# Optimization experiments

Measured on AMD Instinct MI355X. Metric: run time of the kernel, lower is better.

## Reference

```python
import jax, jax.numpy as jnp
import numpy as np

B, J, O = 32, 20, 20
D, H, F, L = 256, 8, 1024, 6
S = J * O
DH = D // H
NL = L + 1  # 6 encoder blocks + final block stacked together


def setup_inputs() -> dict:
    ks = jax.random.split(jax.random.key(0), 16)
    s = 0.02
    am = jax.random.randint(ks[4], (B, J), 0, 2) == 1
    am = am.at[:, 0].set(False)  # at least one unmasked job per row (avoid all -inf softmax)
    return {
        "operations": jax.random.normal(ks[0], (B, J, O, 2), jnp.float32),
        "job_ops_mask": jax.random.normal(ks[1], (B, J, O, O), jnp.float32),
        "ops_machines_mask": jax.random.normal(ks[2], (B, S, S), jnp.float32),
        "jobs_next_op_idx": jax.random.randint(ks[3], (B, J, 1), 0, O),
        "action_mask": am,
        "qkv_w": jax.random.normal(ks[5], (NL, 3 * D, D), jnp.float32) * s,
        "qkv_b": jnp.zeros((NL, 3 * D), jnp.float32),
        "out_w": jax.random.normal(ks[6], (NL, D, D), jnp.float32) * s,
        "out_b": jnp.zeros((NL, D), jnp.float32),
        "ln1_g": jnp.ones((NL, D), jnp.float32),
        "ln1_b": jnp.zeros((NL, D), jnp.float32),
        "ln2_g": jnp.ones((NL, D), jnp.float32),
        "ln2_b": jnp.zeros((NL, D), jnp.float32),
        "ff1_w": jax.random.normal(ks[7], (NL, F, D), jnp.float32) * s,
        "ff1_b": jnp.zeros((NL, F), jnp.float32),
        "ff2_w": jax.random.normal(ks[8], (NL, D, F), jnp.float32) * s,
        "ff2_b": jnp.zeros((NL, D), jnp.float32),
        "op_emb_w": jax.random.normal(ks[9], (D, 2), jnp.float32) * s,
        "op_emb_b": jnp.zeros((D,), jnp.float32),
        "pol_w": jax.random.normal(ks[10], (1, D), jnp.float32) * s,
        "pol_b": jnp.zeros((1,), jnp.float32),
    }


def _ln(x, g, b):
    m = x.mean(-1, keepdims=True)
    v = ((x - m) ** 2).mean(-1, keepdims=True)
    return (x - m) * jax.lax.rsqrt(v + 1e-5) * g + b


def _mha(x, mask, qw, qb, ow, ob):
    N, Sq, _ = x.shape
    qkv = x @ qw.T + qb
    q, k, v = jnp.split(qkv, 3, axis=-1)
    q = q.reshape(N, Sq, H, DH).transpose(0, 2, 1, 3)
    k = k.reshape(N, Sq, H, DH).transpose(0, 2, 1, 3)
    v = v.reshape(N, Sq, H, DH).transpose(0, 2, 1, 3)
    sc = jnp.einsum("nhqd,nhkd->nhqk", q, k) / jnp.sqrt(jnp.float32(DH))
    sc = sc + mask  # additive float attn mask, broadcast over heads where needed
    a = jax.nn.softmax(sc, axis=-1)
    o = jnp.einsum("nhqk,nhkd->nhqd", a, v).transpose(0, 2, 1, 3).reshape(N, Sq, D)
    return o @ ow.T + ob


def _forward(operations, job_ops_mask, ops_machines_mask, jobs_next_op_idx, action_mask,
             qkv_w, qkv_b, out_w, out_b, ln1_g, ln1_b, ln2_g, ln2_b,
             ff1_w, ff1_b, ff2_w, ff2_b, op_emb_w, op_emb_b, pol_w, pol_b):
    def block(x, mask, i):  # pre-norm TransformerEncoderLayer, gelu, dropout=0
        h = _ln(x, ln1_g[i], ln1_b[i])
        x = x + _mha(h, mask, qkv_w[i], qkv_b[i], out_w[i], out_b[i])
        h = _ln(x, ln2_g[i], ln2_b[i])
        ff = jax.nn.gelu(h @ ff1_w[i].T + ff1_b[i], approximate=False) @ ff2_w[i].T + ff2_b[i]
        return x + ff

    # sinusoidal positional encoding over the operation index
    pos = jnp.arange(O, dtype=jnp.float32)[:, None]
    div = jnp.exp(jnp.arange(0, D, 2, dtype=jnp.float32) * (-np.log(10000.0) / D))
    pe = jnp.stack([jnp.sin(pos * div), jnp.cos(pos * div)], axis=-1).reshape(O, D)
    x = operations @ op_emb_w.T + op_emb_b + pe[None, None]  # (B,J,O,D)

    # ALiBi slopes: 1/x^(i+1), x = 256^(1/H)
    base = (2.0 ** 8) ** (1.0 / H)
    slope = (1.0 / base ** jnp.arange(1, H + 1, dtype=jnp.float32))[None, :, None, None]
    job_mask = job_ops_mask.reshape(B * J, 1, O, O) * slope  # (B*J, H, O, O)
    mach_mask = ops_machines_mask[:, None, :, :]  # (B, 1, S, S), identical across heads

    for i in range(L):
        if i % 2 == 0:  # per-job attention over operations
            x = block(x.reshape(B * J, O, D), job_mask, i).reshape(B, J, O, D)
        else:  # per-machine attention over all operations
            x = block(x.reshape(B, S, D), mach_mask, i).reshape(B, J, O, D)

    idx = jnp.broadcast_to(jobs_next_op_idx[:, :, :, None], (B, J, 1, D))
    nxt = jnp.take_along_axis(x, idx, axis=2)[:, :, 0, :]  # (B, J, D)
    kp = jnp.where(action_mask, -jnp.inf, 0.0)[:, None, None, :]  # key padding mask
    nxt = block(nxt, kp, L)
    logits = (nxt @ pol_w.T + pol_b)[:, :, 0]
    return jnp.where(action_mask, -jnp.inf, logits)


def reference(operations, job_ops_mask, ops_machines_mask, jobs_next_op_idx, action_mask,
              qkv_w, qkv_b, out_w, out_b, ln1_g, ln1_b, ln2_g, ln2_b,
              ff1_w, ff1_b, ff2_w, ff2_b, op_emb_w, op_emb_b, pol_w, pol_b):
    return _forward(operations, job_ops_mask, ops_machines_mask, jobs_next_op_idx, action_mask,
                    qkv_w, qkv_b, out_w, out_b, ln1_g, ln1_b, ln2_g, ln2_b,
                    ff1_w, ff1_b, ff2_w, ff2_b, op_emb_w, op_emb_b, pol_w, pol_b)
```

## Files before the change

### kernel.cpp

```cpp
#include <hip/hip_runtime.h>
#include <math.h>

#define B_  32
#define J_  20
#define O_  20
#define S_  400
#define D_  256
#define H_  8
#define F_  1024
#define L_  6
#define T_  12800
#define T2_ 640

#define NEG_BIG (-1e30f)

typedef __attribute__((ext_vector_type(8))) short short8;
typedef __attribute__((ext_vector_type(4))) float f32x4;

__device__ __forceinline__ short f2b(float f) {
  union { float f; unsigned u; } c; c.f = f;
  unsigned r = (c.u + 0x7FFFu + ((c.u >> 16) & 1u)) >> 16;
  return (short)r;
}
__device__ __forceinline__ float b2f(short s) {
  union { unsigned u; float f; } c;
  c.u = ((unsigned)(unsigned short)s) << 16;
  return c.f;
}
__device__ __forceinline__ unsigned addpk(unsigned a, unsigned b) {
  union { unsigned u; float f; } x, y;
  x.u = a << 16;        y.u = b << 16;        float lo = x.f + y.f;
  x.u = a & 0xffff0000u; y.u = b & 0xffff0000u; float hi = x.f + y.f;
  return (unsigned)(unsigned short)f2b(lo) | ((unsigned)(unsigned short)f2b(hi) << 16);
}
__device__ __forceinline__ void async_copy16(const short* g, short* l) {
  __builtin_amdgcn_global_load_lds(
      (const __attribute__((address_space(1))) void*)g,
      (__attribute__((address_space(3))) void*)l, 16, 0, 0);
}

__global__ __launch_bounds__(256) void k_f2b4(
    const float* __restrict__ s0, short* __restrict__ d0,
    const float* __restrict__ s1, short* __restrict__ d1,
    const float* __restrict__ s2, short* __restrict__ d2,
    const float* __restrict__ s3, short* __restrict__ d3,
    const float* __restrict__ s4, short* __restrict__ d4)
{
  int bid = blockIdx.x;
  const float* src; short* dst; int base;
  if (bid < 672)        { src = s0; dst = d0; base = bid; }
  else if (bid < 896)   { src = s1; dst = d1; base = bid - 672; }
  else if (bid < 1792)  { src = s2; dst = d2; base = bid - 896; }
  else if (bid < 2688)  { src = s3; dst = d3; base = bid - 1792; }
  else                  { src = s4; dst = d4; base = bid - 2688; }
  int i = (base * 256 + threadIdx.x) * 8;
  float4 a = *(const float4*)(src + i);
  float4 b = *(const float4*)(src + i + 4);
  short8 o;
  o[0] = f2b(a.x); o[1] = f2b(a.y); o[2] = f2b(a.z); o[3] = f2b(a.w);
  o[4] = f2b(b.x); o[5] = f2b(b.y); o[6] = f2b(b.z); o[7] = f2b(b.w);
  *(short8*)(dst + i) = o;
}

__global__ __launch_bounds__(640) void k_maskconv(
    const void* __restrict__ am_raw, int* __restrict__ am_out)
{
  __shared__ int isInt32;
  const int tid = threadIdx.x;
  if (tid == 0) isInt32 = 1;
  __syncthreads();
  if (tid < 160) {
    int v = ((const int*)am_raw)[tid];
    if (v != 0 && v != 1) atomicAnd(&isInt32, 0);
  }
  __syncthreads();
  if (tid < 640) {
    int v;
    if (isInt32) v = ((const int*)am_raw)[tid] != 0;
    else         v = ((const unsigned char*)am_raw)[tid] != 0;
    am_out[tid] = v;
  }
}

__global__ __launch_bounds__(256) void k_embed(
    const float* __restrict__ ops, const float* __restrict__ ew,
    const float* __restrict__ eb, short* __restrict__ x)
{
  int idx = blockIdx.x * 256 + threadIdx.x;
  int d = idx & 255;
  int t = idx >> 8;
  int o = t % O_;
  float a0 = ops[(size_t)t * 2 + 0], a1 = ops[(size_t)t * 2 + 1];
  int k = d >> 1;
  float div = expf((float)(2 * k) * -0.03597789207803197f);
  float ang = (float)o * div;
  float pe = (d & 1) ? cosf(ang) : sinf(ang);
  x[idx] = f2b(a0 * ew[d * 2 + 0] + a1 * ew[d * 2 + 1] + eb[d] + pe);
}

__global__ __launch_bounds__(256) void k_ln(
    const short* __restrict__ x, const float* __restrict__ g, const float* __restrict__ b,
    short* __restrict__ out, int nTok)
{
  int gid = blockIdx.x * 256 + threadIdx.x;
  int tok = gid >> 6, lane = threadIdx.x & 63;
  if (tok >= nTok) return;
  int2 pk = ((const int2*)(x + (size_t)tok * 256))[lane];
  union { unsigned u; float f; } c;
  float vx, vy, vz, vw;
  c.u = (unsigned)pk.x << 16;        vx = c.f;
  c.u = (unsigned)pk.x & 0xffff0000u; vy = c.f;
  c.u = (unsigned)pk.y << 16;        vz = c.f;
  c.u = (unsigned)pk.y & 0xffff0000u; vw = c.f;
  float s = vx + vy + vz + vw;
  #pragma unroll
  for (int off = 32; off > 0; off >>= 1) s += __shfl_down(s, off);
  float mean = __shfl(s, 0) * (1.f / 256.f);
  float dx = vx - mean, dy = vy - mean, dz = vz - mean, dw = vw - mean;
  float q = dx * dx + dy * dy + dz * dz + dw * dw;
  #pragma unroll
  for (int off = 32; off > 0; off >>= 1) q += __shfl_down(q, off);
  float var = __shfl(q, 0) * (1.f / 256.f);
  float inv = 1.f / sqrtf(var + 1e-5f);
  float4 gv = ((const float4*)g)[lane];
  float4 bv = ((const float4*)b)[lane];
  float ox = dx * inv * gv.x + bv.x;
  float oy = dy * inv * gv.y + bv.y;
  float oz = dz * inv * gv.z + bv.z;
  float ow = dw * inv * gv.w + bv.w;
  int2 po;
  po.x = (int)(unsigned short)f2b(ox) | ((int)(unsigned short)f2b(oy) << 16);
  po.y = (int)(unsigned short)f2b(oz) | ((int)(unsigned short)f2b(ow) << 16);
  ((int2*)(out + (size_t)tok * 256))[lane] = po;
}

__global__ __launch_bounds__(256) void k_gemm_bf16(
    const short* __restrict__ A, const short* __restrict__ W,
    const float* __restrict__ bias, const short* __restrict__ R,
    short* __restrict__ C, int M, int N, int K, int act)
{
  __shared__ short LDS_[32768];
  short* Csf = LDS_;
  const int tid  = threadIdx.x;
  const int lane = tid & 63;
  const int wv   = tid >> 6;
  const int lm   = lane & 15;
  const int quad = lane >> 4;
  const int wm   = (wv >> 1) * 64;
  const int wn   = (wv & 1) * 64;
  const int n0 = blockIdx.x * 128;
  const int m0 = blockIdx.y * 128;

  f32x4 acc[4][4] = {};

#define GB_STAGE(buf, kk)                                                      \
  { _Pragma("unroll")                                                          \
    for (int i = 0; i < 4; ++i) {                                              \
      const int c    = tid + 256 * i;                       \
      const int row  = c >> 3;                                     \
      const int kc8  = ((c & 7) ^ (row & 7)) * 8;                              \
      async_copy16(A + (size_t)(m0 + row) * K + (kk) + kc8,                    \
                   &LDS_[(buf) * 16384 + c * 8]);                              \
      async_copy16(W + (size_t)(n0 + row) * K + (kk) + kc8,                    \
                   &LDS_[(buf) * 16384 + 8192 + c * 8]);                       \
    } }

  GB_STAGE(0, 0)
  __syncthreads();

  const int nIter = K >> 6;
  for (int t = 0; t < nIter; ++t) {
    const int cur = t & 1;
    if (t + 1 < nIter) GB_STAGE(cur ^ 1, (t + 1) << 6)
    const short* Asf = &LDS_[cur * 16384];
    const short* Bsf = &LDS_[cur * 16384 + 8192];
    #pragma unroll
    for (int kh = 0; kh < 2; ++kh) {
      short8 af[4], bf[4];
      #pragma unroll
      for (int i = 0; i < 4; ++i) {
        const int row  = wm + i * 16 + lm;
        const int slot = (kh * 4 + quad) ^ (lm & 7);
        af[i] = *(short8*)&Asf[(row * 8 + slot) * 8];
      }
      #pragma unroll
      for (int j = 0; j < 4; ++j) {
        const int row  = wn + j * 16 + lm;
        const int slot = (kh * 4 + quad) ^ (lm & 7);
        bf[j] = *(short8*)&Bsf[(row * 8 + slot) * 8];
      }
      #pragma unroll
      for (int i = 0; i < 4; ++i)
        #pragma unroll
        for (int j = 0; j < 4; ++j)
          acc[i][j] = __builtin_amdgcn_mfma_f32_16x16x32_bf16(af[i], bf[j], acc[i][j], 0, 0, 0);
    }
    __syncthreads();
  }
#undef GB_STAGE

  #pragma unroll
  for (int j = 0; j < 4; ++j) {
    const int ccol = wn + j * 16 + lm;
    const float bv = bias[n0 + ccol];
    #pragma unroll
    for (int i = 0; i < 4; ++i) {
      #pragma unroll
      for (int r = 0; r < 4; ++r) {
        const int row = wm + i * 16 + quad * 4 + r;
        float vvv = acc[i][j][r] + bv;
        if (act) vvv = vvv / (1.f + __expf(-1.702f * vvv));
        Csf[row * 136 + ccol] = f2b(vvv);
      }
    }
  }
  __syncthreads();
  {
    const int srow = tid >> 1, sh = (tid & 1) * 64;
    const size_t gbase = (size_t)(m0 + srow) * N + n0 + sh;
    const short* ls = &Csf[srow * 136 + sh];
    #pragma unroll
    for (int u = 0; u < 8; ++u) {
      uint4 v = *(const uint4*)(ls + u * 8);
      if (R) {
        uint4 rv = *(const uint4*)(R + gbase + u * 8);
        v.x = addpk(v.x, rv.x); v.y = addpk(v.y, rv.y);
        v.z = addpk(v.z, rv.z); v.w = addpk(v.w, rv.w);
      }
      *(uint4*)(C + gbase + u * 8) = v;
    }
  }
}

__global__ __launch_bounds__(256) void k_gemm_ln(
    const short* __restrict__ A, const short* __restrict__ W,
    const float* __restrict__ bias, const short* __restrict__ R,
    short* __restrict__ X, short* __restrict__ Hout,
    const float* __restrict__ g, const float* __restrict__ bb_,
    int M, int K)
{
  __shared__ short LDS_[40960];
  short* Csf = LDS_;
  const int tid  = threadIdx.x;
  const int lane = tid & 63;
  const int wv   = tid >> 6;
  const int lm   = lane & 15;
  const int quad = lane >> 4;
  const int wn   = wv * 64;
  const int m0   = blockIdx.x * 64;

  f32x4 acc[4][4] = {};

#define GL_STAGE(buf, kk)                                                      \
  { _Pragma("unroll")                                                          \
    for (int i = 0; i < 2; ++i) {                           \
      const int c   = tid + 256 * i;                                           \
      const int row = c >> 3;                                                  \
      const int kc8 = ((c & 7) ^ (row & 7)) * 8;                               \
      async_copy16(A + (size_t)(m0 + row) * K + (kk) + kc8,                    \
                   &LDS_[(buf) * 20480 + c * 8]);                              \
    }                                                                          \
    _Pragma("unroll")                                                          \
    for (int i = 0; i < 8; ++i) {           \
      const int c   = tid + 256 * i;                                           \
      const int row = c >> 3;                                                  \
      const int kc8 = ((c & 7) ^ (row & 7)) * 8;                               \
      async_copy16(W + (size_t)row * K + (kk) + kc8,                           \
                   &LDS_[(buf) * 20480 + 4096 + c * 8]);                       \
    } }

  GL_STAGE(0, 0)
  __syncthreads();

  const int nIter = K >> 6;
  for (int t = 0; t < nIter; ++t) {
    const int cur = t & 1;
    if (t + 1 < nIter) GL_STAGE(cur ^ 1, (t + 1) << 6)
    const short* Asf = &LDS_[cur * 20480];
    const short* Bsf = &LDS_[cur * 20480 + 4096];
    #pragma unroll
    for (int kh = 0; kh < 2; ++kh) {
      short8 af[4], bf[4];
      #pragma unroll
      for (int i = 0; i < 4; ++i) {
        const int row  = i * 16 + lm;
        const int slot = (kh * 4 + quad) ^ (lm & 7);
        af[i] = *(short8*)&Asf[(row * 8 + slot) * 8];
      }
      #pragma unroll
      for (int j = 0; j < 4; ++j) {
        const int row  = wn + j * 16 + lm;
        const int slot = (kh * 4 + quad) ^ (lm & 7);
        bf[j] = *(short8*)&Bsf[(row * 8 + slot) * 8];
      }
      #pragma unroll
      for (int i = 0; i < 4; ++i)
        #pragma unroll
        for (int j = 0; j < 4; ++j)
          acc[i][j] = __builtin_amdgcn_mfma_f32_16x16x32_bf16(af[i], bf[j], acc[i][j], 0, 0, 0);
    }
    __syncthreads();
  }
#undef GL_STAGE

  #pragma unroll
  for (int j = 0; j < 4; ++j) {
    const int ccol = wn + j * 16 + lm;
    const float bv = bias[ccol];
    #pragma unroll
    for (int i = 0; i < 4; ++i) {
      #pragma unroll
      for (int r = 0; r < 4; ++r) {
        const int row = i * 16 + quad * 4 + r;
        Csf[row * 264 + ccol] = f2b(acc[i][j][r] + bv);
      }
    }
  }
  __syncthreads();

  {
    const int row = tid >> 2, cb = (tid & 3) * 64;
    const size_t gbase = (size_t)(m0 + row) * 256 + cb;
    const short* ls = &Csf[row * 264 + cb];
    uint4 xv[8];
    float s1 = 0.f, s2 = 0.f;
    #pragma unroll
    for (int u = 0; u < 8; ++u) {
      uint4 v = *(const uint4*)(ls + u * 8);
      uint4 rv = *(const uint4*)(R + gbase + u * 8);
      v.x = addpk(v.x, rv.x); v.y = addpk(v.y, rv.y);
      v.z = addpk(v.z, rv.z); v.w = addpk(v.w, rv.w);
      xv[u] = v;
      *(uint4*)(X + gbase + u * 8) = v;
      #pragma unroll
      for (int w2 = 0; w2 < 4; ++w2) {
        unsigned pv = (&v.x)[w2];
        union { unsigned u; float f; } c1, c2;
        c1.u = pv << 16; c2.u = pv & 0xffff0000u;
        s1 += c1.f + c2.f;
        s2 += c1.f * c1.f + c2.f * c2.f;
      }
    }
    s1 += __shfl_xor(s1, 1); s2 += __shfl_xor(s2, 1);
    s1 += __shfl_xor(s1, 2); s2 += __shfl_xor(s2, 2);
    const float mean = s1 * (1.f / 256.f);
    const float var  = s2 * (1.f / 256.f) - mean * mean;
    const float inv  = 1.f / sqrtf(var + 1e-5f);
    #pragma unroll
    for (int u = 0; u < 8; ++u) {
      float4 g0 = *(const float4*)(g + cb + u * 8);
      float4 g1 = *(const float4*)(g + cb + u * 8 + 4);
      float4 b0 = *(const float4*)(bb_ + cb + u * 8);
      float4 b1 = *(const float4*)(bb_ + cb + u * 8 + 4);
      auto lnpk = [&](unsigned pv, float ga, float gb2, float ba, float bb2) -> unsigned {
        union { unsigned u; float f; } c1, c2;
        c1.u = pv << 16; c2.u = pv & 0xffff0000u;
        float lo = (c1.f - mean) * inv * ga + ba;
        float hi = (c2.f - mean) * inv * gb2 + bb2;
        return (unsigned)(unsigned short)f2b(lo) | ((unsigned)(unsigned short)f2b(hi) << 16);
      };
      uint4 hv;
      hv.x = lnpk(xv[u].x, g0.x, g0.y, b0.x, b0.y);
      hv.y = lnpk(xv[u].y, g0.z, g0.w, b0.z, b0.w);
      hv.z = lnpk(xv[u].z, g1.x, g1.y, b1.x, b1.y);
      hv.w = lnpk(xv[u].w, g1.z, g1.w, b1.z, b1.w);
      *(uint4*)(Hout + gbase + u * 8) = hv;
    }
  }
}

#define QSTR 776
#define PSTR20 40
__global__ __launch_bounds__(512) void k_attn20_mfma(
    const short* __restrict__ qkv, short* __restrict__ att,
    const float* __restrict__ jmask, const int* __restrict__ amask, int mode)
{
  __shared__ short QK[32 * QSTR];
  __shared__ short Ps[8][32 * PSTR20];
  const int seq  = blockIdx.x;
  const int tid  = threadIdx.x;
  const int wv   = tid >> 6;
  const int lane = tid & 63;
  const int l15  = lane & 15;
  const int quad = lane >> 4;
  const float scale = 0.1767766952966369f;

  for (int e = tid; e < 3072; e += 512) {
    int row = e / 96, c8 = (e % 96) * 8;
    uint4 v = {0u, 0u, 0u, 0u};
    if (row < 20) v = *(const uint4*)(qkv + ((size_t)seq * 20 + row) * 768 + c8);
    *(uint4*)&QK[row * QSTR + c8] = v;
  }
  __syncthreads();

  const short8 aq0 = *(short8*)&QK[(0  + l15) * QSTR + wv * 32 + quad * 8];
  const short8 aq1 = *(short8*)&QK[(16 + l15) * QSTR + wv * 32 + quad * 8];
  const short8 bk0 = *(short8*)&QK[(0  + l15) * QSTR + 256 + wv * 32 + quad * 8];
  const short8 bk1 = *(short8*)&QK[(16 + l15) * QSTR + 256 + wv * 32 + quad * 8];
  f32x4 z4 = {0.f, 0.f, 0.f, 0.f};
  f32x4 s00 = __builtin_amdgcn_mfma_f32_16x16x32_bf16(aq0, bk0, z4, 0, 0, 0);
  f32x4 s01 = __builtin_amdgcn_mfma_f32_16x16x32_bf16(aq0, bk1, z4, 0, 0, 0);
  f32x4 s10 = __builtin_amdgcn_mfma_f32_16x16x32_bf16(aq1, bk0, z4, 0, 0, 0);
  f32x4 s11 = __builtin_amdgcn_mfma_f32_16x16x32_bf16(aq1, bk1, z4, 0, 0, 0);

  const float slope = exp2f(-(float)(wv + 1));
  short* psw = &Ps[wv][0];
  float l0[4] = {0.f, 0.f, 0.f, 0.f};
  float l1[4] = {0.f, 0.f, 0.f, 0.f};

  #pragma unroll
  for (int kt = 0; kt < 2; ++kt) {
    const int k  = kt * 16 + l15;
    const int kc = (k < 20) ? k : 19;
    float madd1 = 0.f;
    if (mode == 1) madd1 = amask[seq * 20 + kc] ? NEG_BIG : 0.f;
    #pragma unroll
    for (int qt = 0; qt < 2; ++qt) {
      f32x4 s = (kt == 0) ? (qt == 0 ? s00 : s10) : (qt == 0 ? s01 : s11);
      #pragma unroll
      for (int r = 0; r < 4; ++r) {
        const int q  = qt * 16 + quad * 4 + r;
        const int qc = (q < 20) ? q : 19;
        float sv = s[r] * scale;
        if (mode == 0) sv += jmask[(size_t)seq * 400 + qc * 20 + kc] * slope;
        else           sv += madd1;
        float p = (k < 20) ? __expf(fminf(sv, 40.f)) : 0.f;
        if (qt == 0) l0[r] += p; else l1[r] += p;
        psw[q * PSTR20 + k] = f2b(p);
      }
    }
  }
  #pragma unroll
  for (int r = 0; r < 4; ++r) {
    float t0 = l0[r];
    t0 += __shfl_xor(t0, 1); t0 += __shfl_xor(t0, 2);
    t0 += __shfl_xor(t0, 4); t0 += __shfl_xor(t0, 8);
    l0[r] = 1.f / t0;
    float t1 = l1[r];
    t1 += __shfl_xor(t1, 1); t1 += __shfl_xor(t1, 2);
    t1 += __shfl_xor(t1, 4); t1 += __shfl_xor(t1, 8);
    l1[r] = 1.f / t1;
  }

  const short8 pf0 = *(short8*)&psw[(0  + l15) * PSTR20 + quad * 8];
  const short8 pf1 = *(short8*)&psw[(16 + l15) * PSTR20 + quad * 8];
  #pragma unroll
  for (int dt = 0; dt < 2; ++dt) {
    const int d = wv * 32 + dt * 16 + l15;
    short8 vf;
    #pragma unroll
    for (int j = 0; j < 8; ++j)
      vf[j] = QK[(quad * 8 + j) * QSTR + 512 + d];
    f32x4 o0 = __builtin_amdgcn_mfma_f32_16x16x32_bf16(pf0, vf, z4, 0, 0, 0);
    f32x4 o1 = __builtin_amdgcn_mfma_f32_16x16x32_bf16(pf1, vf, z4, 0, 0, 0);
    #pragma unroll
    for (int r = 0; r < 4; ++r) {
      const int q = quad * 4 + r;
      att[((size_t)seq * 20 + q) * 256 + d] = f2b(o0[r] * l0[r]);
    }
    if (quad == 0) {
      #pragma unroll
      for (int r = 0; r < 4; ++r) {
        const int q = 16 + r;
        att[((size_t)seq * 20 + q) * 256 + d] = f2b(o1[r] * l1[r]);
      }
    }
  }
}

#define VTS 416
__global__ __launch_bounds__(256) void k_vtrans(
    const short* __restrict__ qkv, short* __restrict__ vt)
{
  __shared__ short T[64][73];
  const int bid = blockIdx.x;
  const int b  = bid / 28, rem = bid % 28;
  const int kt = rem / 4, dt = rem % 4;
  const int k0 = kt * 64, d0 = dt * 64;
  const int tid = threadIdx.x;
  #pragma unroll
  for (int i = 0; i < 2; ++i) {
    const int c = tid + 256 * i;
    const int row = c >> 3, cc = (c & 7) * 8;
    const int tok = k0 + row;
    uint4 v = {0u, 0u, 0u, 0u};
    if (tok < 400)
      v = *(const uint4*)(qkv + ((size_t)(b * 400 + tok)) * 768 + 512 + d0 + cc);
    *(uint4*)&T[row][cc] = v;
  }
  __syncthreads();
  #pragma unroll
  for (int i = 0; i < 2; ++i) {
    const int c = tid + 256 * i;
    const int dl = c >> 3, kk = (c & 7) * 8;
    if (k0 + kk < VTS) {
      short8 o;
      #pragma unroll
      for (int j = 0; j < 8; ++j) o[j] = T[kk + j][dl];
      *(short8*)(vt + ((size_t)(b * 256 + d0 + dl)) * VTS + k0 + kk) = o;
    }
  }
}

#define PSTRW 40
#define MSTR 424
__global__ __launch_bounds__(512) void k_attn400_mfma(
    const short* __restrict__ qkv, const short* __restrict__ vt,
    short* __restrict__ att, const short* __restrict__ mbf)
{
  __shared__ short Pl[8][2 * 16 * PSTRW];
  __shared__ short Ml[32 * MSTR];

  const int id   = blockIdx.x;
  const int b    = (id & 7) + 8 * ((id >> 3) / 13);
  const int qt   = (id >> 3) % 13;
  const int tid  = threadIdx.x;
  const int wv   = tid >> 6;
  const int lane = tid & 63;
  const int l15  = lane & 15;
  const int quad = lane >> 4;
  const int q0   = qt * 32;
  const float scale = 0.1767766952966369f;

  for (int e = tid; e < 32 * 52; e += 512) {
    const int row = e / 52, cc = e % 52;
    const int srow = (q0 + row < 400) ? (q0 + row) : 399;
    uint4 v = {0u, 0u, 0u, 0u};
    if (cc < 50)
      v = *(const uint4*)(mbf + ((size_t)(b * 400 + srow)) * 400 + cc * 8);
    *(uint4*)&Ml[row * MSTR + cc * 8] = v;
  }

  short* Pw0 = &Pl[wv][0];
  short* Pw1 = &Pl[wv][16 * PSTRW];
  const short* qbase = qkv + (size_t)b * 400 * 768;
  const short* vtb   = vt + ((size_t)b * 256 + wv * 32) * VTS;

  const short8 af0 = *(const short8*)(qbase + (size_t)(q0 + l15) * 768 + wv * 32 + quad * 8);
  int aq1 = q0 + 16 + l15; if (aq1 > 399) aq1 = 399;
  const short8 af1 = *(const short8*)(qbase + (size_t)aq1 * 768 + wv * 32 + quad * 8);

  f32x4 accO[2][2] = {};
  float lsum0 = 0.f, lsum1 = 0.f;

  short8 kA0, kA1, vA0, vA1, kB0, kB1, vB0, vB1;

#define PREFKV(K0, KF0, KF1, VF0, VF1)                                          \
  {                                                                             \
    KF0 = *(const short8*)(qbase + (size_t)((K0) + l15) * 768 + 256 + wv * 32 + quad * 8); \
    int kr_ = (K0) + 16 + l15; if (kr_ > 399) kr_ = 399;                        \
    KF1 = *(const short8*)(qbase + (size_t)kr_ * 768 + 256 + wv * 32 + quad * 8); \
    VF0 = *(const short8*)(vtb + (size_t)(0  + l15) * VTS + (K0) + quad * 8);   \
    VF1 = *(const short8*)(vtb + (size_t)(16 + l15) * VTS + (K0) + quad * 8);   \
  }

#define BODY(K0, KF0, KF1, VF0, VF1)                                            \
  {                                                                             \
    f32x4 z4 = {0.f, 0.f, 0.f, 0.f};                                            \
    f32x4 s00 = __builtin_amdgcn_mfma_f32_16x16x32_bf16(KF0, af0, z4, 0, 0, 0); \
    f32x4 s01 = __builtin_amdgcn_mfma_f32_16x16x32_bf16(KF1, af0, z4, 0, 0, 0); \
    f32x4 s10 = __builtin_amdgcn_mfma_f32_16x16x32_bf16(KF0, af1, z4, 0, 0, 0); \
    f32x4 s11 = __builtin_amdgcn_mfma_f32_16x16x32_bf16(KF1, af1, z4, 0, 0, 0); \
    const short* mr0 = &Ml[l15 * MSTR];                                         \
    const short* mr1 = &Ml[(16 + l15) * MSTR];                                  \
    uint2 ma0 = *(const uint2*)(mr0 + (K0) + quad * 4);                         \
    uint2 mb0 = *(const uint2*)(mr0 + (K0) + 16 + quad * 4);                    \
    uint2 ma1 = *(const uint2*)(mr1 + (K0) + quad * 4);                         \
    uint2 mb1 = *(const uint2*)(mr1 + (K0) + 16 + quad * 4);                    \
    float p00[4], p01[4], p10[4], p11[4];                                       \
    _Pragma("unroll")                                                           \
    for (int r = 0; r < 4; ++r) {                                               \
      const int kB = (K0) + 16 + quad * 4 + r;                                  \
      union { unsigned u; float f; } cm;                                        \
      unsigned wa0 = (r < 2) ? ma0.x : ma0.y;                                   \
      unsigned wb0 = (r < 2) ? mb0.x : mb0.y;                                   \
      unsigned wa1 = (r < 2) ? ma1.x : ma1.y;                                   \
      unsigned wb1 = (r < 2) ? mb1.x : mb1.y;                                   \
      cm.u = (r & 1) ? (wa0 & 0xffff0000u) : (wa0 << 16); float mA0 = cm.f;     \
      cm.u = (r & 1) ? (wb0 & 0xffff0000u) : (wb0 << 16); float mB0 = cm.f;     \
      cm.u = (r & 1) ? (wa1 & 0xffff0000u) : (wa1 << 16); float mA1 = cm.f;     \
      cm.u = (r & 1) ? (wb1 & 0xffff0000u) : (wb1 << 16); float mB1 = cm.f;     \
      float sA0 = s00[r] * scale + mA0;                                         \
      float sB0 = (kB < 400) ? (s01[r] * scale + mB0) : NEG_BIG;                \
      float sA1 = s10[r] * scale + mA1;                                         \
      float sB1 = (kB < 400) ? (s11[r] * scale + mB1) : NEG_BIG;                \
      p00[r] = __expf(fminf(sA0, 40.f));                                        \
      p01[r] = __expf(fminf(sB0, 40.f));                                        \
      p10[r] = __expf(fminf(sA1, 40.f));                                        \
      p11[r] = __expf(fminf(sB1, 40.f));                                        \
      lsum0 += p00[r] + p01[r];                                                 \
      lsum1 += p10[r] + p11[r];                                                 \
    }                                                                           \
    unsigned q00, q01, q02, q03, q10, q11, q12, q13;                            \
    asm("v_cvt_pk_bf16_f32 %0, %1, %2" : "=v"(q00) : "v"(p00[0]), "v"(p00[1]));  \
    asm("v_cvt_pk_bf16_f32 %0, %1, %2" : "=v"(q01) : "v"(p00[2]), "v"(p00[3]));  \
    asm("v_cvt_pk_bf16_f32 %0, %1, %2" : "=v"(q02) : "v"(p01[0]), "v"(p01[1]));  \
    asm("v_cvt_pk_bf16_f32 %0, %1, %2" : "=v"(q03) : "v"(p01[2]), "v"(p01[3]));  \
    asm("v_cvt_pk_bf16_f32 %0, %1, %2" : "=v"(q10) : "v"(p10[0]), "v"(p10[1]));  \
    asm("v_cvt_pk_bf16_f32 %0, %1, %2" : "=v"(q11) : "v"(p10[2]), "v"(p10[3]));  \
    asm("v_cvt_pk_bf16_f32 %0, %1, %2" : "=v"(q12) : "v"(p11[0]), "v"(p11[1]));  \
    asm("v_cvt_pk_bf16_f32 %0, %1, %2" : "=v"(q13) : "v"(p11[2]), "v"(p11[3]));  \
    uint2 w00; w00.x = q00; w00.y = q01;                                        \
    uint2 w01; w01.x = q02; w01.y = q03;                                        \
    uint2 w10; w10.x = q10; w10.y = q11;                                        \
    uint2 w11; w11.x = q12; w11.y = q13;                                        \
    *(uint2*)&Pw0[l15 * PSTRW + quad * 4]      = w00;                           \
    *(uint2*)&Pw0[l15 * PSTRW + 16 + quad * 4] = w01;                           \
    *(uint2*)&Pw1[l15 * PSTRW + quad * 4]      = w10;                           \
    *(uint2*)&Pw1[l15 * PSTRW + 16 + quad * 4] = w11;                           \
    const short8 pf0 = *(short8*)&Pw0[l15 * PSTRW + quad * 8];                  \
    const short8 pf1 = *(short8*)&Pw1[l15 * PSTRW + quad * 8];                  \
    accO[0][0] = __builtin_amdgcn_mfma_f32_16x16x32_bf16(VF0, pf0, accO[0][0], 0, 0, 0); \
    accO[0][1] = __builtin_amdgcn_mfma_f32_16x16x32_bf16(VF1, pf0, accO[0][1], 0, 0, 0); \
    accO[1][0] = __builtin_amdgcn_mfma_f32_16x16x32_bf16(VF0, pf1, accO[1][0], 0, 0, 0); \
    accO[1][1] = __builtin_amdgcn_mfma_f32_16x16x32_bf16(VF1, pf1, accO[1][1], 0, 0, 0); \
  }

  PREFKV(0, kA0, kA1, vA0, vA1)
  PREFKV(32, kB0, kB1, vB0, vB1)

  __syncthreads();

  int k0 = 0;
  #pragma unroll 1
  for (int it = 0; it < 6; ++it) {
    BODY(k0, kA0, kA1, vA0, vA1)
    if (k0 + 64 < 416) PREFKV(k0 + 64, kA0, kA1, vA0, vA1)
    k0 += 32;
    BODY(k0, kB0, kB1, vB0, vB1)
    if (k0 + 64 < 416) PREFKV(k0 + 64, kB0, kB1, vB0, vB1)
    k0 += 32;
  }
  BODY(k0, kA0, kA1, vA0, vA1)

#undef PREFKV
#undef BODY

  lsum0 += __shfl_xor(lsum0, 16);
  lsum0 += __shfl_xor(lsum0, 32);
  lsum1 += __shfl_xor(lsum1, 16);
  lsum1 += __shfl_xor(lsum1, 32);
  const float inv0 = 1.f / lsum0;
  const float inv1 = 1.f / lsum1;

  #pragma unroll
  for (int qh = 0; qh < 2; ++qh) {
    const int q = q0 + qh * 16 + l15;
    if (q >= 400) continue;
    const float inv = qh ? inv1 : inv0;
    #pragma unroll
    for (int c = 0; c < 2; ++c) {
      float a0 = accO[qh][c][0] * inv, a1 = accO[qh][c][1] * inv;
      float a2 = accO[qh][c][2] * inv, a3 = accO[qh][c][3] * inv;
      unsigned o01, o23;
      asm("v_cvt_pk_bf16_f32 %0, %1, %2" : "=v"(o01) : "v"(a0), "v"(a1));
      asm("v_cvt_pk_bf16_f32 %0, %1, %2" : "=v"(o23) : "v"(a2), "v"(a3));
      uint2 ov; ov.x = o01; ov.y = o23;
      *(uint2*)&att[((size_t)b * 400 + q) * 256 + wv * 32 + c * 16 + quad * 4] = ov;
    }
  }
}

__global__ __launch_bounds__(256) void k_gather2(
    const short* __restrict__ x, const short* __restrict__ h,
    const int* __restrict__ idx, short* __restrict__ x2, short* __restrict__ h2)
{
  int t = blockIdx.x * 256 + threadIdx.x;
  if (t >= 640 * 16) return;
  int bj = t >> 4, c = t & 15;
  int o = idx[bj];
  size_t src = ((size_t)bj * 20 + o) * 256;
  ((uint4*)(x2 + (size_t)bj * 256))[c] = ((const uint4*)(x + src))[c];
  ((uint4*)(h2 + (size_t)bj * 256))[c] = ((const uint4*)(h + src))[c];
}

__global__ __launch_bounds__(256) void k_logits(
    const short* __restrict__ x2, const float* __restrict__ pw, const float* __restrict__ pb,
    const int* __restrict__ am, float* __restrict__ out)
{
  int gid = blockIdx.x * 256 + threadIdx.x;
  int row = gid >> 6, lane = threadIdx.x & 63;
  int2 pk = ((const int2*)(x2 + (size_t)row * 256))[lane];
  union { unsigned u; float f; } c;
  float vx, vy, vz, vw;
  c.u = (unsigned)pk.x << 16;         vx = c.f;
  c.u = (unsigned)pk.x & 0xffff0000u; vy = c.f;
  c.u = (unsigned)pk.y << 16;         vz = c.f;
  c.u = (unsigned)pk.y & 0xffff0000u; vw = c.f;
  float4 w = ((const float4*)pw)[lane];
  float s = vx * w.x + vy * w.y + vz * w.z + vw * w.w;
  #pragma unroll
  for (int off = 32; off > 0; off >>= 1) s += __shfl_down(s, off);
  if (lane == 0) out[row] = am[row] ? NEG_BIG : (s + pb[0]);
}

extern "C" void kernel_launch(void* const* d_in, const int* in_sizes, int n_in,
                              void* d_out, int out_size, void* d_ws, size_t ws_size,
                              hipStream_t stream)
{
  (void)in_sizes; (void)n_in; (void)out_size; (void)ws_size;
  const float* operations        = (const float*)d_in[0];
  const float* job_ops_mask      = (const float*)d_in[1];
  const float* ops_machines_mask = (const float*)d_in[2];
  const int*   jobs_next_op_idx  = (const int*)d_in[3];
  const void*  action_mask_raw   = (const void*)d_in[4];
  const float* qkv_w = (const float*)d_in[5];
  const float* qkv_b = (const float*)d_in[6];
  const float* out_w = (const float*)d_in[7];
  const float* out_b = (const float*)d_in[8];
  const float* ln1_g = (const float*)d_in[9];
  const float* ln1_b = (const float*)d_in[10];
  const float* ln2_g = (const float*)d_in[11];
  const float* ln2_b = (const float*)d_in[12];
  const float* ff1_w = (const float*)d_in[13];
  const float* ff1_b = (const float*)d_in[14];
  const float* ff2_w = (const float*)d_in[15];
  const float* ff2_b = (const float*)d_in[16];
  const float* op_emb_w = (const float*)d_in[17];
  const float* op_emb_b = (const float*)d_in[18];
  const float* pol_w = (const float*)d_in[19];
  const float* pol_b = (const float*)d_in[20];
  float* out = (float*)d_out;

  short* x    = (short*)d_ws;
  short* x2   = x + (size_t)T_ * D_;
  short* h    = x2 + (size_t)T2_ * D_;
  short* big  = h + (size_t)T_ * D_;
  short* h2   = big + (size_t)T_ * F_;
  short* big2 = h2 + (size_t)T2_ * D_;
  int*   amc  = (int*)(big2 + (size_t)T2_ * F_);
  short* bwq  = (short*)(amc + 640);
  short* bwo  = bwq + (size_t)7 * 768 * 256;
  short* bwf1 = bwo + (size_t)7 * 256 * 256;
  short* bwf2 = bwf1 + (size_t)7 * 1024 * 256;
  short* mbf  = bwf2 + (size_t)7 * 256 * 1024;
  short* vt   = mbf + (size_t)B_ * 400 * 400;

  auto gemm = [&](const short* A, const short* Wb, const float* bias, const short* R,
                  short* C, int M, int N, int K, int act) {
    k_gemm_bf16<<<dim3(N / 128, M / 128), dim3(256), 0, stream>>>(
        A, Wb, bias, R, C, M, N, K, act);
  };
  auto gemm_ln = [&](const short* A, const short* Wb, const float* bias, const short* R,
                     short* X, short* Hout, const float* g, const float* b, int M, int K) {
    k_gemm_ln<<<dim3(M / 64), dim3(256), 0, stream>>>(
        A, Wb, bias, R, X, Hout, g, b, M, K);
  };

  k_f2b4<<<dim3(5188), 256, 0, stream>>>(qkv_w, bwq, out_w, bwo, ff1_w, bwf1,
                                         ff2_w, bwf2, ops_machines_mask, mbf);
  k_maskconv<<<dim3(1), dim3(640), 0, stream>>>(action_mask_raw, amc);
  k_embed<<<dim3(T_ * D_ / 256), dim3(256), 0, stream>>>(operations, op_emb_w, op_emb_b, x);
  k_ln<<<dim3(T_ / 4), 256, 0, stream>>>(x, ln1_g, ln1_b, h, T_);

  for (int i = 0; i < L_; ++i) {
    const short* qw  = bwq  + (size_t)i * 768 * 256;
    const float* qb  = qkv_b + (size_t)i * 768;
    const short* ow  = bwo  + (size_t)i * 256 * 256;
    const float* ob  = out_b + (size_t)i * 256;
    const short* f1w = bwf1 + (size_t)i * 1024 * 256;
    const float* f1b = ff1_b + (size_t)i * 1024;
    const short* f2w = bwf2 + (size_t)i * 256 * 1024;
    const float* f2b_ = ff2_b + (size_t)i * 256;
    gemm(h, qw, qb, nullptr, big, T_, 768, 256, 0);
    if ((i & 1) == 0) {
      k_attn20_mfma<<<dim3(640), 512, 0, stream>>>(big, h, job_ops_mask, nullptr, 0);
    } else {
      k_vtrans<<<dim3(896), 256, 0, stream>>>(big, vt);
      k_attn400_mfma<<<dim3(416), 512, 0, stream>>>(big, vt, h, mbf);
    }
    gemm_ln(h, ow, ob, x, x, h, ln2_g + i * D_, ln2_b + i * D_, T_, 256);
    gemm(h, f1w, f1b, nullptr, big, T_, 1024, 256, 1);
    gemm_ln(big, f2w, f2b_, x, x, h, ln1_g + (i + 1) * D_, ln1_b + (i + 1) * D_, T_, 1024);
  }

  k_gather2<<<dim3(40), 256, 0, stream>>>(x, h, jobs_next_op_idx, x2, h2);

  {
    int i = L_;
    const short* qw  = bwq  + (size_t)i * 768 * 256;
    const float* qb  = qkv_b + (size_t)i * 768;
    const short* ow  = bwo  + (size_t)i * 256 * 256;
    const float* ob  = out_b + (size_t)i * 256;
    const short* f1w = bwf1 + (size_t)i * 1024 * 256;
    const float* f1b = ff1_b + (size_t)i * 1024;
    const short* f2w = bwf2 + (size_t)i * 256 * 1024;
    const float* f2b_ = ff2_b + (size_t)i * 256;
    gemm(h2, qw, qb, nullptr, big2, T2_, 768, 256, 0);
    k_attn20_mfma<<<dim3(32), 512, 0, stream>>>(big2, h2, nullptr, amc, 1);
    gemm_ln(h2, ow, ob, x2, x2, h2, ln2_g + i * D_, ln2_b + i * D_, T2_, 256);
    gemm(h2, f1w, f1b, nullptr, big2, T2_, 1024, 256, 1);
    gemm(big2, f2w, f2b_, x2, x2, T2_, 256, 1024, 0);
  }

  k_logits<<<dim3(160), 256, 0, stream>>>(x2, pol_w, pol_b, amc, out);
}
```

Baseline: 876.7 us.

## Repartition 400-token attention to one block per batch-head with K/V staged in LDS

```diff
diff --git a/kernel.cpp b/kernel.cpp
--- a/kernel.cpp
+++ b/kernel.cpp
@@ -502,161 +502,148 @@
   }
 }
 
+#define KSTR  36
+#define VSTRL 436
 #define PSTRW 40
-#define MSTR 424
 __global__ __launch_bounds__(512) void k_attn400_mfma(
     const short* __restrict__ qkv, const short* __restrict__ vt,
     short* __restrict__ att, const short* __restrict__ mbf)
 {
+  __shared__ short Kl[416 * KSTR];
+  __shared__ short Vl[32 * VSTRL];
   __shared__ short Pl[8][2 * 16 * PSTRW];
-  __shared__ short Ml[32 * MSTR];
 
   const int id   = blockIdx.x;
-  const int b    = (id & 7) + 8 * ((id >> 3) / 13);
-  const int qt   = (id >> 3) % 13;
+  const int b    = id & 31;
+  const int hd   = id >> 5;
   const int tid  = threadIdx.x;
   const int wv   = tid >> 6;
   const int lane = tid & 63;
   const int l15  = lane & 15;
   const int quad = lane >> 4;
-  const int q0   = qt * 32;
   const float scale = 0.1767766952966369f;
 
-  for (int e = tid; e < 32 * 52; e += 512) {
-    const int row = e / 52, cc = e % 52;
-    const int srow = (q0 + row < 400) ? (q0 + row) : 399;
-    uint4 v = {0u, 0u, 0u, 0u};
-    if (cc < 50)
-      v = *(const uint4*)(mbf + ((size_t)(b * 400 + srow)) * 400 + cc * 8);
-    *(uint4*)&Ml[row * MSTR + cc * 8] = v;
-  }
+  const short* qbase = qkv + (size_t)b * 400 * 768;
+  const short* kgl   = qbase + 256 + hd * 32;
+  const short* vtb   = vt + ((size_t)b * 256 + hd * 32) * VTS;
+
+  for (int e = tid; e < 1664; e += 512) {
+    const int row = e >> 2, seg = e & 3;
+    const int rs = row < 400 ? row : 399;
+    uint4 v = *(const uint4*)(kgl + (size_t)rs * 768 + seg * 8);
+    *(uint4*)&Kl[row * KSTR + seg * 8] = v;
+  }
+  for (int e = tid; e < 1664; e += 512) {
+    const int row = e / 52, seg = e % 52;
+    uint4 v = *(const uint4*)(vtb + (size_t)row * VTS + seg * 8);
+    *(uint4*)&Vl[row * VSTRL + seg * 8] = v;
+  }
+  __syncthreads();
 
   short* Pw0 = &Pl[wv][0];
   short* Pw1 = &Pl[wv][16 * PSTRW];
-  const short* qbase = qkv + (size_t)b * 400 * 768;
-  const short* vtb   = vt + ((size_t)b * 256 + wv * 32) * VTS;
-
-  const short8 af0 = *(const short8*)(qbase + (size_t)(q0 + l15) * 768 + wv * 32 + quad * 8);
-  int aq1 = q0 + 16 + l15; if (aq1 > 399) aq1 = 399;
-  const short8 af1 = *(const short8*)(qbase + (size_t)aq1 * 768 + wv * 32 + quad * 8);
-
-  f32x4 accO[2][2] = {};
-  float lsum0 = 0.f, lsum1 = 0.f;
-
-  short8 kA0, kA1, vA0, vA1, kB0, kB1, vB0, vB1;
-
-#define PREFKV(K0, KF0, KF1, VF0, VF1)                                          \
-  {                                                                             \
-    KF0 = *(const short8*)(qbase + (size_t)((K0) + l15) * 768 + 256 + wv * 32 + quad * 8); \
-    int kr_ = (K0) + 16 + l15; if (kr_ > 399) kr_ = 399;                        \
-    KF1 = *(const short8*)(qbase + (size_t)kr_ * 768 + 256 + wv * 32 + quad * 8); \
-    VF0 = *(const short8*)(vtb + (size_t)(0  + l15) * VTS + (K0) + quad * 8);   \
-    VF1 = *(const short8*)(vtb + (size_t)(16 + l15) * VTS + (K0) + quad * 8);   \
-  }
-
-#define BODY(K0, KF0, KF1, VF0, VF1)                                            \
-  {                                                                             \
-    f32x4 z4 = {0.f, 0.f, 0.f, 0.f};                                            \
-    f32x4 s00 = __builtin_amdgcn_mfma_f32_16x16x32_bf16(KF0, af0, z4, 0, 0, 0); \
-    f32x4 s01 = __builtin_amdgcn_mfma_f32_16x16x32_bf16(KF1, af0, z4, 0, 0, 0); \
-    f32x4 s10 = __builtin_amdgcn_mfma_f32_16x16x32_bf16(KF0, af1, z4, 0, 0, 0); \
-    f32x4 s11 = __builtin_amdgcn_mfma_f32_16x16x32_bf16(KF1, af1, z4, 0, 0, 0); \
-    const short* mr0 = &Ml[l15 * MSTR];                                         \
-    const short* mr1 = &Ml[(16 + l15) * MSTR];                                  \
-    uint2 ma0 = *(const uint2*)(mr0 + (K0) + quad * 4);                         \
-    uint2 mb0 = *(const uint2*)(mr0 + (K0) + 16 + quad * 4);                    \
-    uint2 ma1 = *(const uint2*)(mr1 + (K0) + quad * 4);                         \
-    uint2 mb1 = *(const uint2*)(mr1 + (K0) + 16 + quad * 4);                    \
-    float p00[4], p01[4], p10[4], p11[4];                                       \
-    _Pragma("unroll")                                                           \
-    for (int r = 0; r < 4; ++r) {                                               \
-      const int kB = (K0) + 16 + quad * 4 + r;                                  \
-      union { unsigned u; float f; } cm;                                        \
-      unsigned wa0 = (r < 2) ? ma0.x : ma0.y;                                   \
-      unsigned wb0 = (r < 2) ? mb0.x : mb0.y;                                   \
-      unsigned wa1 = (r < 2) ? ma1.x : ma1.y;                                   \
-      unsigned wb1 = (r < 2) ? mb1.x : mb1.y;                                   \
-      cm.u = (r & 1) ? (wa0 & 0xffff0000u) : (wa0 << 16); float mA0 = cm.f;     \
-      cm.u = (r & 1) ? (wb0 & 0xffff0000u) : (wb0 << 16); float mB0 = cm.f;     \
-      cm.u = (r & 1) ? (wa1 & 0xffff0000u) : (wa1 << 16); float mA1 = cm.f;     \
-      cm.u = (r & 1) ? (wb1 & 0xffff0000u) : (wb1 << 16); float mB1 = cm.f;     \
-      float sA0 = s00[r] * scale + mA0;                                         \
-      float sB0 = (kB < 400) ? (s01[r] * scale + mB0) : NEG_BIG;                \
-      float sA1 = s10[r] * scale + mA1;                                         \
-      float sB1 = (kB < 400) ? (s11[r] * scale + mB1) : NEG_BIG;                \
-      p00[r] = __expf(fminf(sA0, 40.f));                                        \
-      p01[r] = __expf(fminf(sB0, 40.f));                                        \
-      p10[r] = __expf(fminf(sA1, 40.f));                                        \
-      p11[r] = __expf(fminf(sB1, 40.f));                                        \
-      lsum0 += p00[r] + p01[r];                                                 \
-      lsum1 += p10[r] + p11[r];                                                 \
-    }                                                                           \
-    unsigned q00, q01, q02, q03, q10, q11, q12, q13;                            \
-    asm("v_cvt_pk_bf16_f32 %0, %1, %2" : "=v"(q00) : "v"(p00[0]), "v"(p00[1]));  \
-    asm("v_cvt_pk_bf16_f32 %0, %1, %2" : "=v"(q01) : "v"(p00[2]), "v"(p00[3]));  \
-    asm("v_cvt_pk_bf16_f32 %0, %1, %2" : "=v"(q02) : "v"(p01[0]), "v"(p01[1]));  \
-    asm("v_cvt_pk_bf16_f32 %0, %1, %2" : "=v"(q03) : "v"(p01[2]), "v"(p01[3]));  \
-    asm("v_cvt_pk_bf16_f32 %0, %1, %2" : "=v"(q10) : "v"(p10[0]), "v"(p10[1]));  \
-    asm("v_cvt_pk_bf16_f32 %0, %1, %2" : "=v"(q11) : "v"(p10[2]), "v"(p10[3]));  \
-    asm("v_cvt_pk_bf16_f32 %0, %1, %2" : "=v"(q12) : "v"(p11[0]), "v"(p11[1]));  \
-    asm("v_cvt_pk_bf16_f32 %0, %1, %2" : "=v"(q13) : "v"(p11[2]), "v"(p11[3]));  \
-    uint2 w00; w00.x = q00; w00.y = q01;                                        \
-    uint2 w01; w01.x = q02; w01.y = q03;                                        \
-    uint2 w10; w10.x = q10; w10.y = q11;                                        \
-    uint2 w11; w11.x = q12; w11.y = q13;                                        \
-    *(uint2*)&Pw0[l15 * PSTRW + quad * 4]      = w00;                           \
-    *(uint2*)&Pw0[l15 * PSTRW + 16 + quad * 4] = w01;                           \
-    *(uint2*)&Pw1[l15 * PSTRW + quad * 4]      = w10;                           \
-    *(uint2*)&Pw1[l15 * PSTRW + 16 + quad * 4] = w11;                           \
-    const short8 pf0 = *(short8*)&Pw0[l15 * PSTRW + quad * 8];                  \
-    const short8 pf1 = *(short8*)&Pw1[l15 * PSTRW + quad * 8];                  \
-    accO[0][0] = __builtin_amdgcn_mfma_f32_16x16x32_bf16(VF0, pf0, accO[0][0], 0, 0, 0); \
-    accO[0][1] = __builtin_amdgcn_mfma_f32_16x16x32_bf16(VF1, pf0, accO[0][1], 0, 0, 0); \
-    accO[1][0] = __builtin_amdgcn_mfma_f32_16x16x32_bf16(VF0, pf1, accO[1][0], 0, 0, 0); \
-    accO[1][1] = __builtin_amdgcn_mfma_f32_16x16x32_bf16(VF1, pf1, accO[1][1], 0, 0, 0); \
-  }
-
-  PREFKV(0, kA0, kA1, vA0, vA1)
-  PREFKV(32, kB0, kB1, vB0, vB1)
-
-  __syncthreads();
-
-  int k0 = 0;
-  #pragma unroll 1
-  for (int it = 0; it < 6; ++it) {
-    BODY(k0, kA0, kA1, vA0, vA1)
-    if (k0 + 64 < 416) PREFKV(k0 + 64, kA0, kA1, vA0, vA1)
-    k0 += 32;
-    BODY(k0, kB0, kB1, vB0, vB1)
-    if (k0 + 64 < 416) PREFKV(k0 + 64, kB0, kB1, vB0, vB1)
-    k0 += 32;
-  }
-  BODY(k0, kA0, kA1, vA0, vA1)
-
-#undef PREFKV
-#undef BODY
-
-  lsum0 += __shfl_xor(lsum0, 16);
-  lsum0 += __shfl_xor(lsum0, 32);
-  lsum1 += __shfl_xor(lsum1, 16);
-  lsum1 += __shfl_xor(lsum1, 32);
-  const float inv0 = 1.f / lsum0;
-  const float inv1 = 1.f / lsum1;
-
-  #pragma unroll
-  for (int qh = 0; qh < 2; ++qh) {
-    const int q = q0 + qh * 16 + l15;
-    if (q >= 400) continue;
-    const float inv = qh ? inv1 : inv0;
-    #pragma unroll
-    for (int c = 0; c < 2; ++c) {
-      float a0 = accO[qh][c][0] * inv, a1 = accO[qh][c][1] * inv;
-      float a2 = accO[qh][c][2] * inv, a3 = accO[qh][c][3] * inv;
-      unsigned o01, o23;
-      asm("v_cvt_pk_bf16_f32 %0, %1, %2" : "=v"(o01) : "v"(a0), "v"(a1));
-      asm("v_cvt_pk_bf16_f32 %0, %1, %2" : "=v"(o23) : "v"(a2), "v"(a3));
-      uint2 ov; ov.x = o01; ov.y = o23;
-      *(uint2*)&att[((size_t)b * 400 + q) * 256 + wv * 32 + c * 16 + quad * 4] = ov;
+
+  for (int tile = wv; tile < 13; tile += 8) {
+    const int q0 = tile * 32;
+    const short8 af0 = *(const short8*)(qbase + (size_t)(q0 + l15) * 768 + hd * 32 + quad * 8);
+    int aq1 = q0 + 16 + l15; if (aq1 > 399) aq1 = 399;
+    const short8 af1 = *(const short8*)(qbase + (size_t)aq1 * 768 + hd * 32 + quad * 8);
+    const short* mr0 = mbf + (size_t)(b * 400 + q0 + l15) * 400;
+    const short* mr1 = mbf + (size_t)(b * 400 + aq1) * 400;
+
+    f32x4 accO[2][2] = {};
+    float lsum0 = 0.f, lsum1 = 0.f;
+
+    #pragma unroll
+    for (int k0 = 0; k0 < 416; k0 += 32) {
+      const short8 kf0 = *(const short8*)&Kl[(k0 + l15) * KSTR + quad * 8];
+      const short8 kf1 = *(const short8*)&Kl[(k0 + 16 + l15) * KSTR + quad * 8];
+      f32x4 z4 = {0.f, 0.f, 0.f, 0.f};
+      f32x4 s00 = __builtin_amdgcn_mfma_f32_16x16x32_bf16(kf0, af0, z4, 0, 0, 0);
+      f32x4 s01 = __builtin_amdgcn_mfma_f32_16x16x32_bf16(kf1, af0, z4, 0, 0, 0);
+      f32x4 s10 = __builtin_amdgcn_mfma_f32_16x16x32_bf16(kf0, af1, z4, 0, 0, 0);
+      f32x4 s11 = __builtin_amdgcn_mfma_f32_16x16x32_bf16(kf1, af1, z4, 0, 0, 0);
+
+      uint2 ma0 = *(const uint2*)(mr0 + k0 + quad * 4);
+      uint2 mb0 = *(const uint2*)(mr0 + k0 + 16 + quad * 4);
+      uint2 ma1 = *(const uint2*)(mr1 + k0 + quad * 4);
+      uint2 mb1 = *(const uint2*)(mr1 + k0 + 16 + quad * 4);
+
+      float p00[4], p01[4], p10[4], p11[4];
+      #pragma unroll
+      for (int r = 0; r < 4; ++r) {
+        const int kB = k0 + 16 + quad * 4 + r;
+        union { unsigned u; float f; } cm;
+        unsigned wa0 = (r < 2) ? ma0.x : ma0.y;
+        unsigned wb0 = (r < 2) ? mb0.x : mb0.y;
+        unsigned wa1 = (r < 2) ? ma1.x : ma1.y;
+        unsigned wb1 = (r < 2) ? mb1.x : mb1.y;
+        cm.u = (r & 1) ? (wa0 & 0xffff0000u) : (wa0 << 16); float mA0 = cm.f;
+        cm.u = (r & 1) ? (wb0 & 0xffff0000u) : (wb0 << 16); float mB0 = cm.f;
+        cm.u = (r & 1) ? (wa1 & 0xffff0000u) : (wa1 << 16); float mA1 = cm.f;
+        cm.u = (r & 1) ? (wb1 & 0xffff0000u) : (wb1 << 16); float mB1 = cm.f;
+        float sA0 = s00[r] * scale + mA0;
+        float sB0 = (kB < 400) ? (s01[r] * scale + mB0) : NEG_BIG;
+        float sA1 = s10[r] * scale + mA1;
+        float sB1 = (kB < 400) ? (s11[r] * scale + mB1) : NEG_BIG;
+        p00[r] = __expf(fminf(sA0, 40.f));
+        p01[r] = __expf(fminf(sB0, 40.f));
+        p10[r] = __expf(fminf(sA1, 40.f));
+        p11[r] = __expf(fminf(sB1, 40.f));
+        lsum0 += p00[r] + p01[r];
+        lsum1 += p10[r] + p11[r];
+      }
+
+      unsigned q00, q01, q02, q03, q10, q11, q12, q13;
+      asm("v_cvt_pk_bf16_f32 %0, %1, %2" : "=v"(q00) : "v"(p00[0]), "v"(p00[1]));
+      asm("v_cvt_pk_bf16_f32 %0, %1, %2" : "=v"(q01) : "v"(p00[2]), "v"(p00[3]));
+      asm("v_cvt_pk_bf16_f32 %0, %1, %2" : "=v"(q02) : "v"(p01[0]), "v"(p01[1]));
+      asm("v_cvt_pk_bf16_f32 %0, %1, %2" : "=v"(q03) : "v"(p01[2]), "v"(p01[3]));
+      asm("v_cvt_pk_bf16_f32 %0, %1, %2" : "=v"(q10) : "v"(p10[0]), "v"(p10[1]));
+      asm("v_cvt_pk_bf16_f32 %0, %1, %2" : "=v"(q11) : "v"(p10[2]), "v"(p10[3]));
+      asm("v_cvt_pk_bf16_f32 %0, %1, %2" : "=v"(q12) : "v"(p11[0]), "v"(p11[1]));
+      asm("v_cvt_pk_bf16_f32 %0, %1, %2" : "=v"(q13) : "v"(p11[2]), "v"(p11[3]));
+      uint2 w00; w00.x = q00; w00.y = q01;
+      uint2 w01; w01.x = q02; w01.y = q03;
+      uint2 w10; w10.x = q10; w10.y = q11;
+      uint2 w11; w11.x = q12; w11.y = q13;
+      *(uint2*)&Pw0[l15 * PSTRW + quad * 4]      = w00;
+      *(uint2*)&Pw0[l15 * PSTRW + 16 + quad * 4] = w01;
+      *(uint2*)&Pw1[l15 * PSTRW + quad * 4]      = w10;
+      *(uint2*)&Pw1[l15 * PSTRW + 16 + quad * 4] = w11;
+      const short8 pf0 = *(short8*)&Pw0[l15 * PSTRW + quad * 8];
+      const short8 pf1 = *(short8*)&Pw1[l15 * PSTRW + quad * 8];
+
+      const short8 vf0 = *(const short8*)&Vl[l15 * VSTRL + k0 + quad * 8];
+      const short8 vf1 = *(const short8*)&Vl[(16 + l15) * VSTRL + k0 + quad * 8];
+      accO[0][0] = __builtin_amdgcn_mfma_f32_16x16x32_bf16(vf0, pf0, accO[0][0], 0, 0, 0);
+      accO[0][1] = __builtin_amdgcn_mfma_f32_16x16x32_bf16(vf1, pf0, accO[0][1], 0, 0, 0);
+      accO[1][0] = __builtin_amdgcn_mfma_f32_16x16x32_bf16(vf0, pf1, accO[1][0], 0, 0, 0);
+      accO[1][1] = __builtin_amdgcn_mfma_f32_16x16x32_bf16(vf1, pf1, accO[1][1], 0, 0, 0);
+    }
+
+    lsum0 += __shfl_xor(lsum0, 16);
+    lsum0 += __shfl_xor(lsum0, 32);
+    lsum1 += __shfl_xor(lsum1, 16);
+    lsum1 += __shfl_xor(lsum1, 32);
+    const float inv0 = 1.f / lsum0;
+    const float inv1 = 1.f / lsum1;
+
+    #pragma unroll
+    for (int qh = 0; qh < 2; ++qh) {
+      const int q = q0 + qh * 16 + l15;
+      if (q >= 400) continue;
+      const float inv = qh ? inv1 : inv0;
+      #pragma unroll
+      for (int c = 0; c < 2; ++c) {
+        float a0 = accO[qh][c][0] * inv, a1 = accO[qh][c][1] * inv;
+        float a2 = accO[qh][c][2] * inv, a3 = accO[qh][c][3] * inv;
+        unsigned o01, o23;
+        asm("v_cvt_pk_bf16_f32 %0, %1, %2" : "=v"(o01) : "v"(a0), "v"(a1));
+        asm("v_cvt_pk_bf16_f32 %0, %1, %2" : "=v"(o23) : "v"(a2), "v"(a3));
+        uint2 ov; ov.x = o01; ov.y = o23;
+        *(uint2*)&att[((size_t)b * 400 + q) * 256 + hd * 32 + c * 16 + quad * 4] = ov;
+      }
     }
   }
 }
@@ -767,7 +754,7 @@
       k_attn20_mfma<<<dim3(640), 512, 0, stream>>>(big, h, job_ops_mask, nullptr, 0);
     } else {
       k_vtrans<<<dim3(896), 256, 0, stream>>>(big, vt);
-      k_attn400_mfma<<<dim3(416), 512, 0, stream>>>(big, vt, h, mbf);
+      k_attn400_mfma<<<dim3(256), 512, 0, stream>>>(big, vt, h, mbf);
     }
     gemm_ln(h, ow, ob, x, x, h, ln2_g + i * D_, ln2_b + i * D_, T_, 256);
     gemm(h, f1w, f1b, nullptr, big, T_, 1024, 256, 1);
```

After: 868.4 us. About the same (-0.9%).
